# Kernel optimization log

Measured on AMD Instinct MI355X. Metric: run time of the kernel, lower is better.

Reference implementation:

```python
import jax, jax.numpy as jnp
import numpy as np

N, D, H, E, TOP_K = 8192, 1024, 2048, 8, 2


def setup_inputs() -> dict:
    key = jax.random.key(0)
    ks = jax.random.split(key, 5)
    s_in = 1.0 / np.sqrt(D)
    s_hid = 1.0 / np.sqrt(H)
    return {
        "x": jax.random.normal(ks[0], (N, D), dtype=jnp.float32),
        "Wg": jax.random.normal(ks[1], (D, E), dtype=jnp.float32) * s_in,
        "bg": jnp.zeros((E,), dtype=jnp.float32),
        "W1": jax.random.normal(ks[2], (E, D, H), dtype=jnp.float32) * s_in,
        "b1": jnp.zeros((E, H), dtype=jnp.float32),
        "W2": jax.random.normal(ks[3], (E, H, H), dtype=jnp.float32) * s_hid,
        "b2": jnp.zeros((E, H), dtype=jnp.float32),
    }


def _moe_forward(x, Wg, bg, W1, b1, W2, b2):
    # Router
    gate_logits = x @ Wg + bg                      # [N, E]
    gate_probs = jax.nn.softmax(gate_logits, axis=-1)
    topk_probs, topk_idx = jax.lax.top_k(gate_probs, TOP_K)  # [N, K]
    topk_probs = topk_probs / (jnp.sum(topk_probs, axis=-1, keepdims=True) + 1e-8)
    rows = jnp.arange(x.shape[0])[:, None]
    gate_mask = jnp.zeros_like(gate_probs).at[rows, topk_idx].set(topk_probs)  # [N, E]

    # Dense all-expert compute (dropout is identity in eval)
    h = jax.nn.relu(jnp.einsum('nd,edh->neh', x, W1) + b1)    # [N, E, H]
    expert_out = jnp.einsum('neh,ehk->nek', h, W2) + b2        # [N, E, H]

    output = jnp.einsum('neh,ne->nh', expert_out, gate_mask)   # [N, H]
    return output, gate_probs, gate_mask


def reference(x, Wg, bg, W1, b1, W2, b2):
    return _moe_forward(x, Wg, bg, W1, b1, W2, b2)
```

## Files before the change

### kernel.cpp

```cpp
#include <hip/hip_runtime.h>

#define N_TOK 8192
#define DIM   1024
#define HID   2048
#define NEXP  8
#define TOPK  2
#define BM 256
#define BN 256
#define BK 64
#define NTHREADS 512
#define MAXROWS (N_TOK*TOPK + NEXP*BM)
#define MAXRT   (MAXROWS/BM)
#define NT_COL  (HID/BN)
#define NPAIR   (N_TOK*TOPK)

typedef float f32x4 __attribute__((ext_vector_type(4)));
typedef short bf16x8 __attribute__((ext_vector_type(8)));

static __device__ __forceinline__ unsigned short f2bf(float f){
    union { float f; unsigned u; } v; v.f = f;
    unsigned r = v.u + 0x7FFFu + ((v.u >> 16) & 1u);
    return (unsigned short)(r >> 16);
}
static __device__ __forceinline__ float bf2f(unsigned short u){
    union { unsigned u; float f; } v; v.u = ((unsigned)u) << 16;
    return v.f;
}

static __device__ __forceinline__ void gload_lds16(const void* g, void* l){
    __builtin_amdgcn_global_load_lds((const __attribute__((address_space(1))) void*)g,
                                     (__attribute__((address_space(3))) void*)l,
                                     16, 0, 0);
}

__global__ __launch_bounds__(256) void cvt_transpose_moe(
    const float* __restrict__ src, unsigned short* __restrict__ dst, int R, int C)
{
    __shared__ float tile[64][65];
    const size_t plane = (size_t)R * C;
    const float* s = src + (size_t)blockIdx.z * plane;
    unsigned short* d = dst + (size_t)blockIdx.z * plane;
    const int c0 = blockIdx.x * 64, r0 = blockIdx.y * 64;
    const int tq = threadIdx.x & 15, tr = threadIdx.x >> 4;
    #pragma unroll
    for (int p = 0; p < 4; ++p) {
        int row = p*16 + tr;
        float4 v = *(const float4*)(s + (size_t)(r0 + row) * C + c0 + tq*4);
        tile[row][tq*4+0] = v.x; tile[row][tq*4+1] = v.y;
        tile[row][tq*4+2] = v.z; tile[row][tq*4+3] = v.w;
    }
    __syncthreads();
    #pragma unroll
    for (int p = 0; p < 4; ++p) {
        int orow = p*16 + tr;
        ushort4 o;
        o.x = f2bf(tile[tq*4+0][orow]);
        o.y = f2bf(tile[tq*4+1][orow]);
        o.z = f2bf(tile[tq*4+2][orow]);
        o.w = f2bf(tile[tq*4+3][orow]);
        *(ushort4*)(d + (size_t)(c0 + orow) * R + r0 + tq*4) = o;
    }
}

__global__ __launch_bounds__(256) void router_moe(
    const float* __restrict__ x, const float* __restrict__ Wg, const float* __restrict__ bg,
    float* __restrict__ gate_probs, float* __restrict__ gate_mask,
    int* __restrict__ tk_e, float* __restrict__ tk_w)
{
    const int lane = threadIdx.x & 63;
    const int n = blockIdx.x * 4 + (threadIdx.x >> 6);
    const float* xr = x + (size_t)n * DIM;

    float acc[NEXP];
    #pragma unroll
    for (int e = 0; e < NEXP; ++e) acc[e] = 0.f;
    #pragma unroll 4
    for (int i = 0; i < DIM/64; ++i) {
        int d = i*64 + lane;
        float xv = xr[d];
        const float4* wrow = (const float4*)(Wg + (size_t)d * NEXP);
        float4 w0 = wrow[0], w1 = wrow[1];
        acc[0] += xv*w0.x; acc[1] += xv*w0.y; acc[2] += xv*w0.z; acc[3] += xv*w0.w;
        acc[4] += xv*w1.x; acc[5] += xv*w1.y; acc[6] += xv*w1.z; acc[7] += xv*w1.w;
    }
    #pragma unroll
    for (int off = 32; off > 0; off >>= 1) {
        #pragma unroll
        for (int e = 0; e < NEXP; ++e) acc[e] += __shfl_xor(acc[e], off, 64);
    }
    float lgt[NEXP];
    float mx = acc[0] + bg[0];
    #pragma unroll
    for (int e = 0; e < NEXP; ++e) { lgt[e] = acc[e] + bg[e]; mx = fmaxf(mx, lgt[e]); }
    float s = 0.f;
    #pragma unroll
    for (int e = 0; e < NEXP; ++e) { lgt[e] = expf(lgt[e] - mx); s += lgt[e]; }
    float inv = 1.f / s;
    #pragma unroll
    for (int e = 0; e < NEXP; ++e) lgt[e] *= inv;

    int i1 = 0;
    #pragma unroll
    for (int e = 1; e < NEXP; ++e) if (lgt[e] > lgt[i1]) i1 = e;
    int i2 = (i1 == 0) ? 1 : 0;
    #pragma unroll
    for (int e = 0; e < NEXP; ++e) if (e != i1 && lgt[e] > lgt[i2]) i2 = e;
    float wsum = lgt[i1] + lgt[i2] + 1e-8f;
    float w1n = lgt[i1] / wsum, w2n = lgt[i2] / wsum;

    if (lane < NEXP) {
        gate_probs[(size_t)n*NEXP + lane] = lgt[lane];
        gate_mask [(size_t)n*NEXP + lane] = (lane == i1) ? w1n : (lane == i2) ? w2n : 0.f;
    }
    if (lane == 0) {
        tk_e[n*TOPK]   = i1; tk_e[n*TOPK+1] = i2;
        tk_w[n*TOPK]   = w1n; tk_w[n*TOPK+1] = w2n;
    }
}

__global__ __launch_bounds__(1024) void assign_moe(
    const int* __restrict__ tk_e,
    int* __restrict__ slot_row, int* __restrict__ pair_token,
    int* __restrict__ sched_e, int* __restrict__ sched_row,
    int* __restrict__ total_tiles)
{
    __shared__ int whist[16][NEXP];
    __shared__ int wbase[16][NEXP];
    const int w = threadIdx.x >> 6, lane = threadIdx.x & 63;
    const int PW = NPAIR / 16;
    const unsigned long long below = ((unsigned long long)1 << lane) - 1;

    int h[NEXP] = {0,0,0,0,0,0,0,0};
    for (int i = 0; i < PW/64; ++i) {
        int e = tk_e[w*PW + i*64 + lane];
        #pragma unroll
        for (int ee = 0; ee < NEXP; ++ee)
            h[ee] += __popcll(__ballot(e == ee));
    }
    if (lane == 0) {
        #pragma unroll
        for (int ee = 0; ee < NEXP; ++ee) whist[w][ee] = h[ee];
    }
    __syncthreads();

    if (threadIdx.x == 0) {
        int base = 0, t = 0, ebase[NEXP];
        for (int e = 0; e < NEXP; ++e) {
            int c = 0;
            for (int ww = 0; ww < 16; ++ww) c += whist[ww][e];
            ebase[e] = base;
            int nt = (c + BM - 1) / BM;
            for (int i = 0; i < nt; ++i) { sched_e[t] = e; sched_row[t] = base + i*BM; ++t; }
            base += nt * BM;
        }
        *total_tiles = t;
        for (int e = 0; e < NEXP; ++e) {
            int r = ebase[e];
            for (int ww = 0; ww < 16; ++ww) { wbase[ww][e] = r; r += whist[ww][e]; }
        }
    }
    __syncthreads();

    int run[NEXP];
    #pragma unroll
    for (int ee = 0; ee < NEXP; ++ee) run[ee] = wbase[w][ee];
    for (int i = 0; i < PW/64; ++i) {
        int idx = w*PW + i*64 + lane;
        int e = tk_e[idx];
        int myslot = 0;
        #pragma unroll
        for (int ee = 0; ee < NEXP; ++ee) {
            unsigned long long m = __ballot(e == ee);
            if (e == ee) myslot = run[ee] + __popcll(m & below);
            run[ee] += __popcll(m);
        }
        slot_row[idx] = myslot;
        pair_token[myslot] = idx;
    }
}

__global__ __launch_bounds__(256) void gather_moe(
    const float* __restrict__ x, const int* __restrict__ slot_row,
    unsigned short* __restrict__ Xg)
{
    const int n = blockIdx.x;
    const int r0 = slot_row[n*TOPK], r1 = slot_row[n*TOPK+1];
    float4 xv = ((const float4*)(x + (size_t)n * DIM))[threadIdx.x];
    ushort4 b;
    b.x = f2bf(xv.x); b.y = f2bf(xv.y); b.z = f2bf(xv.z); b.w = f2bf(xv.w);
    ((ushort4*)(Xg + (size_t)r0 * DIM))[threadIdx.x] = b;
    ((ushort4*)(Xg + (size_t)r1 * DIM))[threadIdx.x] = b;
}

#define PHASE_MFMA(MH, NH, BF) do {                                          \
    __builtin_amdgcn_s_setprio(1);                                           \
    _Pragma("unroll")                                                        \
    for (int mi = 0; mi < 4; ++mi)                                           \
        _Pragma("unroll")                                                    \
        for (int nb = 0; nb < 2; ++nb)                                       \
            _Pragma("unroll")                                                \
            for (int kk = 0; kk < 2; ++kk)                                   \
                acc[(MH)*4+mi][(NH)*2+nb] =                                  \
                    __builtin_amdgcn_mfma_f32_16x16x32_bf16(                 \
                        af[mi][kk], BF[nb][kk], acc[(MH)*4+mi][(NH)*2+nb],   \
                        0, 0, 0);                                            \
    __builtin_amdgcn_s_setprio(0);                                           \
} while (0)

template<int K, int MODE>
__global__ __launch_bounds__(512, 1) void gemm_moe(
    const unsigned short* __restrict__ A,
    const unsigned short* __restrict__ Bt,
    const float* __restrict__ bias,
    const int* __restrict__ sched_e, const int* __restrict__ sched_row,
    const int* __restrict__ total_tiles,
    unsigned short* __restrict__ Out,
    const int* __restrict__ pair_token)
{
    const int nwg  = gridDim.x * gridDim.y;
    const int orig = blockIdx.y * gridDim.x + blockIdx.x;
    const int q = nwg >> 3, r8 = nwg & 7, xcd = orig & 7, lin = orig >> 3;
    const int wg = (xcd < r8 ? xcd*(q+1) : r8*(q+1) + (xcd-r8)*q) + lin;
    const int rt = wg / NT_COL, ct = wg % NT_COL;
    if (rt >= *total_tiles) return;

    const int e    = sched_e[rt];
    const int row0 = sched_row[rt];
    const int col0 = ct * BN;
    const unsigned short* Be = Bt + (size_t)e * HID * K;

    __shared__ __align__(1024) char lds[131072];
    char* ldsA = lds;
    char* ldsB = lds + 65536;

    const int tid  = threadIdx.x;
    const int wv   = tid >> 6, lane = tid & 63;
    const int wr   = wv >> 2,  wc   = wv & 3;
    const int lrow = lane & 15, lg  = lane >> 4;
    const int sr   = lane >> 3, si  = lane & 7;
    const int gc16 = si ^ sr;

    const unsigned short* Ab = A  + (size_t)row0 * K + gc16 * 8;
    const unsigned short* Bb = Be + (size_t)col0 * K + gc16 * 8;

    f32x4 acc[8][4] = {};
    bf16x8 af[4][2], b0f[2][2], b1f[2][2];

    auto STAGE_A = [&](int buf, int h, int t) {
        char* dst = ldsA + (buf*2 + h)*16384;
        #pragma unroll
        for (int j = 0; j < 2; ++j) {
            int c = wv*2 + j;
            int r = ((c>>3)<<7) + h*64 + ((c&7)<<3) + sr;
            gload_lds16(Ab + (size_t)r * K + t*BK, dst + c*1024);
        }
    };
    auto STAGE_B = [&](int buf, int h, int t) {
        char* dst = ldsB + (buf*2 + h)*16384;
        #pragma unroll
        for (int j = 0; j < 2; ++j) {
            int c = wv*2 + j;
            int idx = c*8 + sr;
            int gcol = ((idx>>5)<<6) + h*32 + (idx&31);
            gload_lds16(Bb + (size_t)gcol * K + t*BK, dst + c*1024);
        }
    };
    auto RD_A = [&](int buf, int mh) {
        const char* base = ldsA + (buf*2 + mh)*16384;
        #pragma unroll
        for (int mi = 0; mi < 4; ++mi) {
            int idx = wr*64 + mi*16 + lrow;
            #pragma unroll
            for (int kk = 0; kk < 2; ++kk) {
                int s = (kk*4 + lg) ^ (idx & 7);
                af[mi][kk] = *(const bf16x8*)(base + idx*128 + s*16);
            }
        }
    };
    auto RD_B = [&](int buf, int nh, bf16x8 (*bf)[2]) {
        const char* base = ldsB + (buf*2 + nh)*16384;
        #pragma unroll
        for (int nb = 0; nb < 2; ++nb) {
            int idx = wc*32 + nb*16 + lrow;
            #pragma unroll
            for (int kk = 0; kk < 2; ++kk) {
                int s = (kk*4 + lg) ^ (idx & 7);
                bf[nb][kk] = *(const bf16x8*)(base + idx*128 + s*16);
            }
        }
    };
    auto BARRIER = [&]() {
        __builtin_amdgcn_sched_barrier(0);
        __builtin_amdgcn_s_barrier();
        __builtin_amdgcn_sched_barrier(0);
    };
    auto LGKM0 = [&]() {
        asm volatile("s_waitcnt lgkmcnt(0)" ::: "memory");
        __builtin_amdgcn_sched_barrier(0);
    };

    constexpr int NT = K / BK;
    constexpr int NI = NT / 2;
    static_assert(NT % 2 == 0, "even K-tiles required");

    STAGE_A(0,0,0); STAGE_B(0,0,0); STAGE_A(0,1,0); STAGE_B(0,1,0);
    STAGE_A(1,0,1); STAGE_B(1,0,1);
    asm volatile("s_waitcnt vmcnt(4)" ::: "memory");
    BARRIER();

    for (int i = 0; i < NI; ++i) {
        const int ta = 2*i, tb = 2*i + 1;
        const bool pf = (i + 1 < NI);
        RD_A(0,0); RD_B(0,0,b0f);
        STAGE_A(1,1,tb);
        BARRIER(); LGKM0();
        PHASE_MFMA(0,0,b0f);
        BARRIER();
        RD_B(0,1,b1f);
        STAGE_B(1,1,tb);
        BARRIER(); LGKM0();
        PHASE_MFMA(0,1,b1f);
        BARRIER();
        RD_A(0,1);
        if (pf) STAGE_A(0,0,ta+2);
        BARRIER(); LGKM0();
        PHASE_MFMA(1,0,b0f);
        BARRIER();
        if (pf) STAGE_B(0,0,ta+2);
        BARRIER();
        PHASE_MFMA(1,1,b1f);
        if (pf) { asm volatile("s_waitcnt vmcnt(4)" ::: "memory"); }
        else    { asm volatile("s_waitcnt vmcnt(0)" ::: "memory"); }
        BARRIER();
        RD_A(1,0); RD_B(1,0,b0f);
        if (pf) STAGE_A(0,1,ta+2);
        BARRIER(); LGKM0();
        PHASE_MFMA(0,0,b0f);
        BARRIER();
        RD_B(1,1,b1f);
        if (pf) STAGE_B(0,1,ta+2);
        BARRIER(); LGKM0();
        PHASE_MFMA(0,1,b1f);
        BARRIER();
        RD_A(1,1);
        if (pf) STAGE_A(1,0,tb+2);
        BARRIER(); LGKM0();
        PHASE_MFMA(1,0,b0f);
        BARRIER();
        if (pf) STAGE_B(1,0,tb+2);
        BARRIER();
        PHASE_MFMA(1,1,b1f);
        if (pf) { asm volatile("s_waitcnt vmcnt(4)" ::: "memory"); BARRIER(); }
    }

    if constexpr (MODE == 0) {
        #pragma unroll
        for (int nb = 0; nb < 4; ++nb) {
            int col = col0 + wc*64 + nb*16 + lrow;
            float bv = bias[(size_t)e*HID + col];
            #pragma unroll
            for (int mb = 0; mb < 8; ++mb) {
                int rb = row0 + wr*128 + mb*16 + lg*4;
                #pragma unroll
                for (int j = 0; j < 4; ++j) {
                    float v = fmaxf(acc[mb][nb][j] + bv, 0.f);
                    Out[(size_t)(rb + j) * HID + col] = f2bf(v);
                }
            }
        }
    } else {
        float bv[4]; int cols[4];
        #pragma unroll
        for (int nb = 0; nb < 4; ++nb) {
            cols[nb] = col0 + wc*64 + nb*16 + lrow;
            bv[nb] = bias[(size_t)e*HID + cols[nb]];
        }
        #pragma unroll
        for (int mb = 0; mb < 8; ++mb) {
            #pragma unroll
            for (int j = 0; j < 4; ++j) {
                int r = row0 + wr*128 + mb*16 + lg*4 + j;
                int pair = pair_token[r];
                if (pair < 0) continue;
                size_t prow = (size_t)(pair & 1) * N_TOK + (pair >> 1);
                #pragma unroll
                for (int nb = 0; nb < 4; ++nb)
                    Out[prow * HID + cols[nb]] = f2bf(acc[mb][nb][j] + bv[nb]);
            }
        }
    }
}

__global__ __launch_bounds__(256) void combine_moe(
    const unsigned short* __restrict__ P, const float* __restrict__ tk_w,
    float* __restrict__ out)
{
    const int n = blockIdx.x;
    const float w0 = tk_w[n*2], w1 = tk_w[n*2+1];
    const int c = threadIdx.x * 8;
    bf16x8 a = *(const bf16x8*)(P + (size_t)n * HID + c);
    bf16x8 b = *(const bf16x8*)(P + (size_t)(N_TOK + n) * HID + c);
    float4 o0, o1;
    float* op = &o0.x;
    #pragma unroll
    for (int i = 0; i < 4; ++i)
        op[i] = w0 * bf2f((unsigned short)a[i]) + w1 * bf2f((unsigned short)b[i]);
    float* op1 = &o1.x;
    #pragma unroll
    for (int i = 0; i < 4; ++i)
        op1[i] = w0 * bf2f((unsigned short)a[4+i]) + w1 * bf2f((unsigned short)b[4+i]);
    float4* dst = (float4*)(out + (size_t)n * HID + c);
    dst[0] = o0; dst[1] = o1;
}

extern "C" void kernel_launch(void* const* d_in, const int* in_sizes, int n_in,
                              void* d_out, int out_size, void* d_ws, size_t ws_size,
                              hipStream_t stream)
{
    const float* x  = (const float*)d_in[0];
    const float* Wg = (const float*)d_in[1];
    const float* bg = (const float*)d_in[2];
    const float* W1 = (const float*)d_in[3];
    const float* b1 = (const float*)d_in[4];
    const float* W2 = (const float*)d_in[5];
    const float* b2 = (const float*)d_in[6];

    float* out        = (float*)d_out;
    float* gate_probs = out + (size_t)N_TOK * HID;
    float* gate_mask  = gate_probs + (size_t)N_TOK * NEXP;

    char* p = (char*)d_ws;
    auto carve = [&](size_t bytes) { char* r = p; p += (bytes + 255) & ~(size_t)255; return r; };
    unsigned short* W2t = (unsigned short*)carve((size_t)NEXP*HID*HID*2);
    unsigned short* Hb  = (unsigned short*)carve((size_t)MAXROWS*HID*2);
    unsigned short* W1t = (unsigned short*)carve((size_t)NEXP*DIM*HID*2);
    unsigned short* Xg  = (unsigned short*)carve((size_t)MAXROWS*DIM*2);
    unsigned short* P   = W1t;
    int*   pair_token = (int*)  carve((size_t)MAXROWS*4);
    int*   slot_row   = (int*)  carve((size_t)NPAIR*4);
    int*   tk_e       = (int*)  carve((size_t)NPAIR*4);
    float* tk_w       = (float*)carve((size_t)NPAIR*4);
    int*   sched_e    = (int*)  carve(1024);
    int*   sched_row  = (int*)  carve(1024);
    int*   total_tiles= (int*)  carve(256);

    hipMemsetAsync(pair_token, 0xFF, (size_t)MAXROWS*4, stream);

    cvt_transpose_moe<<<dim3(HID/64, DIM/64, NEXP), 256, 0, stream>>>(W1, W1t, DIM, HID);
    cvt_transpose_moe<<<dim3(HID/64, HID/64, NEXP), 256, 0, stream>>>(W2, W2t, HID, HID);
    router_moe<<<N_TOK/4, 256, 0, stream>>>(x, Wg, bg, gate_probs, gate_mask, tk_e, tk_w);
    assign_moe<<<1, 1024, 0, stream>>>(tk_e, slot_row, pair_token,
                                       sched_e, sched_row, total_tiles);
    gather_moe<<<N_TOK, 256, 0, stream>>>(x, slot_row, Xg);
    gemm_moe<DIM, 0><<<dim3(MAXRT, NT_COL), NTHREADS, 0, stream>>>(
        Xg, W1t, b1, sched_e, sched_row, total_tiles, Hb, nullptr);
    gemm_moe<HID, 1><<<dim3(MAXRT, NT_COL), NTHREADS, 0, stream>>>(
        Hb, W2t, b2, sched_e, sched_row, total_tiles, P, pair_token);
    combine_moe<<<N_TOK, 256, 0, stream>>>(P, tk_w, out);
}
```

Baseline: 398.5 us.

## Split first expert GEMM into dedicated 256x128-tile kernel with two blocks per CU

```diff
diff --git a/kernel.cpp b/kernel.cpp
--- a/kernel.cpp
+++ b/kernel.cpp
@@ -6,12 +6,10 @@
 #define NEXP  8
 #define TOPK  2
 #define BM 256
-#define BN 256
 #define BK 64
 #define NTHREADS 512
 #define MAXROWS (N_TOK*TOPK + NEXP*BM)
 #define MAXRT   (MAXROWS/BM)
-#define NT_COL  (HID/BN)
 #define NPAIR   (N_TOK*TOPK)
 
 typedef float f32x4 __attribute__((ext_vector_type(4)));
@@ -192,7 +190,164 @@
     ((ushort4*)(Xg + (size_t)r1 * DIM))[threadIdx.x] = b;
 }
 
-#define PHASE_MFMA(MH, NH, BF) do {                                          \
+#define G1_BN 128
+#define G1_NTCOL (HID/G1_BN)
+
+#define G1_MFMA(MH, NH, BF) do {                                             \
+    __builtin_amdgcn_s_setprio(1);                                           \
+    _Pragma("unroll")                                                        \
+    for (int mi = 0; mi < 2; ++mi)                                           \
+        _Pragma("unroll")                                                    \
+        for (int nb = 0; nb < 2; ++nb)                                       \
+            _Pragma("unroll")                                                \
+            for (int kk = 0; kk < 2; ++kk)                                   \
+                acc[(MH)*2+mi][(NH)*2+nb] =                                  \
+                    __builtin_amdgcn_mfma_f32_16x16x32_bf16(                 \
+                        af[mi][kk], BF[nb][kk], acc[(MH)*2+mi][(NH)*2+nb],   \
+                        0, 0, 0);                                            \
+    __builtin_amdgcn_s_setprio(0);                                           \
+} while (0)
+
+__global__ __launch_bounds__(512, 2) void gemm1_moe(
+    const unsigned short* __restrict__ A,
+    const unsigned short* __restrict__ Bt,
+    const float* __restrict__ bias,
+    const int* __restrict__ sched_e, const int* __restrict__ sched_row,
+    const int* __restrict__ total_tiles,
+    unsigned short* __restrict__ Out)
+{
+    constexpr int K = DIM;
+    const int nwg  = gridDim.x * gridDim.y;
+    const int orig = blockIdx.y * gridDim.x + blockIdx.x;
+    const int q = nwg >> 3, r8 = nwg & 7, xcd = orig & 7, lin = orig >> 3;
+    const int wg = (xcd < r8 ? xcd*(q+1) : r8*(q+1) + (xcd-r8)*q) + lin;
+    const int rt = wg / G1_NTCOL, ct = wg % G1_NTCOL;
+    if (rt >= *total_tiles) return;
+
+    const int e    = sched_e[rt];
+    const int row0 = sched_row[rt];
+    const int col0 = ct * G1_BN;
+    const unsigned short* Be = Bt + (size_t)e * HID * K;
+
+    __shared__ __align__(1024) char lds[49152];
+    char* ldsA = lds;
+    char* ldsB = lds + 32768;
+
+    const int tid  = threadIdx.x;
+    const int wv   = tid >> 6, lane = tid & 63;
+    const int wr   = wv >> 1,  wc   = wv & 1;
+    const int lrow = lane & 15, lg  = lane >> 4;
+    const int sr   = lane >> 3, si  = lane & 7;
+    const int gc16 = si ^ sr;
+
+    const unsigned short* Ab = A  + (size_t)row0 * K + gc16 * 8;
+    const unsigned short* Bb = Be + (size_t)col0 * K + gc16 * 8;
+
+    f32x4 acc[4][4] = {};
+    bf16x8 af[2][2], b0f[2][2], b1f[2][2];
+
+    auto STAGE_A = [&](int h, int t) {
+        char* dst = ldsA + h*16384;
+        #pragma unroll
+        for (int j = 0; j < 2; ++j) {
+            int c = wv*2 + j;
+            int idx = c*8 + sr;
+            int r = ((idx>>5)<<6) + h*32 + (idx&31);
+            gload_lds16(Ab + (size_t)r * K + t*BK, dst + c*1024);
+        }
+    };
+    auto STAGE_B = [&](int h, int t) {
+        char* dst = ldsB + h*8192;
+        int c = wv;
+        int idx = c*8 + sr;
+        int gcol = ((idx>>5)<<6) + h*32 + (idx&31);
+        gload_lds16(Bb + (size_t)gcol * K + t*BK, dst + c*1024);
+    };
+    auto RD_A = [&](int mh) {
+        const char* base = ldsA + mh*16384;
+        #pragma unroll
+        for (int mi = 0; mi < 2; ++mi) {
+            int idx = wr*32 + mi*16 + lrow;
+            #pragma unroll
+            for (int kk = 0; kk < 2; ++kk) {
+                int s = (kk*4 + lg) ^ (idx & 7);
+                af[mi][kk] = *(const bf16x8*)(base + idx*128 + s*16);
+            }
+        }
+    };
+    auto RD_B = [&](int nh, bf16x8 (*bf)[2]) {
+        const char* base = ldsB + nh*8192;
+        #pragma unroll
+        for (int nb = 0; nb < 2; ++nb) {
+            int idx = wc*32 + nb*16 + lrow;
+            #pragma unroll
+            for (int kk = 0; kk < 2; ++kk) {
+                int s = (kk*4 + lg) ^ (idx & 7);
+                bf[nb][kk] = *(const bf16x8*)(base + idx*128 + s*16);
+            }
+        }
+    };
+    auto BARRIER = [&]() {
+        __builtin_amdgcn_sched_barrier(0);
+        __builtin_amdgcn_s_barrier();
+        __builtin_amdgcn_sched_barrier(0);
+    };
+    auto LGKM0 = [&]() {
+        asm volatile("s_waitcnt lgkmcnt(0)" ::: "memory");
+        __builtin_amdgcn_sched_barrier(0);
+    };
+
+    constexpr int NT = K / BK;
+
+    STAGE_A(0, 0); STAGE_B(0, 0); STAGE_B(1, 0); STAGE_A(1, 0);
+    asm volatile("s_waitcnt vmcnt(3)" ::: "memory");
+    BARRIER();
+
+    for (int t = 0; t < NT; ++t) {
+        const bool pf = (t + 1 < NT);
+        RD_A(0); RD_B(0, b0f);
+        BARRIER(); LGKM0();
+        G1_MFMA(0,0,b0f);
+        asm volatile("s_waitcnt vmcnt(2)" ::: "memory");
+        BARRIER();
+        RD_B(1, b1f);
+        if (pf) { STAGE_A(0, t+1); STAGE_B(0, t+1); }
+        BARRIER(); LGKM0();
+        G1_MFMA(0,1,b1f);
+        if (pf) { asm volatile("s_waitcnt vmcnt(3)" ::: "memory"); }
+        else    { asm volatile("s_waitcnt vmcnt(0)" ::: "memory"); }
+        BARRIER();
+        RD_A(1);
+        if (pf) STAGE_B(1, t+1);
+        BARRIER(); LGKM0();
+        G1_MFMA(1,0,b0f);
+        BARRIER();
+        if (pf) STAGE_A(1, t+1);
+        BARRIER();
+        G1_MFMA(1,1,b1f);
+        if (pf) { asm volatile("s_waitcnt vmcnt(3)" ::: "memory"); BARRIER(); }
+    }
+
+    #pragma unroll
+    for (int n = 0; n < 4; ++n) {
+        int col = col0 + wc*64 + ((n>>1)<<5) + ((n&1)<<4) + lrow;
+        float bv = bias[(size_t)e*HID + col];
+        #pragma unroll
+        for (int m = 0; m < 4; ++m) {
+            int rb = row0 + wr*64 + ((m>>1)<<5) + ((m&1)<<4) + lg*4;
+            #pragma unroll
+            for (int j = 0; j < 4; ++j) {
+                float v = fmaxf(acc[m][n][j] + bv, 0.f);
+                Out[(size_t)(rb + j) * HID + col] = f2bf(v);
+            }
+        }
+    }
+}
+
+#define G2_BN 256
+#define G2_NTCOL (HID/G2_BN)
+
+#define G2_MFMA(MH, NH, BF) do {                                             \
     __builtin_amdgcn_s_setprio(1);                                           \
     _Pragma("unroll")                                                        \
     for (int mi = 0; mi < 4; ++mi)                                           \
@@ -207,8 +362,7 @@
     __builtin_amdgcn_s_setprio(0);                                           \
 } while (0)
 
-template<int K, int MODE>
-__global__ __launch_bounds__(512, 1) void gemm_moe(
+__global__ __launch_bounds__(512, 1) void gemm2_moe(
     const unsigned short* __restrict__ A,
     const unsigned short* __restrict__ Bt,
     const float* __restrict__ bias,
@@ -217,16 +371,17 @@
     unsigned short* __restrict__ Out,
     const int* __restrict__ pair_token)
 {
+    constexpr int K = HID;
     const int nwg  = gridDim.x * gridDim.y;
     const int orig = blockIdx.y * gridDim.x + blockIdx.x;
     const int q = nwg >> 3, r8 = nwg & 7, xcd = orig & 7, lin = orig >> 3;
     const int wg = (xcd < r8 ? xcd*(q+1) : r8*(q+1) + (xcd-r8)*q) + lin;
-    const int rt = wg / NT_COL, ct = wg % NT_COL;
+    const int rt = wg / G2_NTCOL, ct = wg % G2_NTCOL;
     if (rt >= *total_tiles) return;
 
     const int e    = sched_e[rt];
     const int row0 = sched_row[rt];
-    const int col0 = ct * BN;
+    const int col0 = ct * G2_BN;
     const unsigned short* Be = Bt + (size_t)e * HID * K;
 
     __shared__ __align__(1024) char lds[131072];
@@ -314,79 +469,62 @@
         RD_A(0,0); RD_B(0,0,b0f);
         STAGE_A(1,1,tb);
         BARRIER(); LGKM0();
-        PHASE_MFMA(0,0,b0f);
+        G2_MFMA(0,0,b0f);
         BARRIER();
         RD_B(0,1,b1f);
         STAGE_B(1,1,tb);
         BARRIER(); LGKM0();
-        PHASE_MFMA(0,1,b1f);
+        G2_MFMA(0,1,b1f);
         BARRIER();
         RD_A(0,1);
         if (pf) STAGE_A(0,0,ta+2);
         BARRIER(); LGKM0();
-        PHASE_MFMA(1,0,b0f);
+        G2_MFMA(1,0,b0f);
         BARRIER();
         if (pf) STAGE_B(0,0,ta+2);
         BARRIER();
-        PHASE_MFMA(1,1,b1f);
+        G2_MFMA(1,1,b1f);
         if (pf) { asm volatile("s_waitcnt vmcnt(4)" ::: "memory"); }
         else    { asm volatile("s_waitcnt vmcnt(0)" ::: "memory"); }
         BARRIER();
         RD_A(1,0); RD_B(1,0,b0f);
         if (pf) STAGE_A(0,1,ta+2);
         BARRIER(); LGKM0();
-        PHASE_MFMA(0,0,b0f);
+        G2_MFMA(0,0,b0f);
         BARRIER();
         RD_B(1,1,b1f);
         if (pf) STAGE_B(0,1,ta+2);
         BARRIER(); LGKM0();
-        PHASE_MFMA(0,1,b1f);
+        G2_MFMA(0,1,b1f);
         BARRIER();
         RD_A(1,1);
         if (pf) STAGE_A(1,0,tb+2);
         BARRIER(); LGKM0();
-        PHASE_MFMA(1,0,b0f);
+        G2_MFMA(1,0,b0f);
         BARRIER();
         if (pf) STAGE_B(1,0,tb+2);
         BARRIER();
-        PHASE_MFMA(1,1,b1f);
+        G2_MFMA(1,1,b1f);
         if (pf) { asm volatile("s_waitcnt vmcnt(4)" ::: "memory"); BARRIER(); }
     }
 
-    if constexpr (MODE == 0) {
-        #pragma unroll
-        for (int nb = 0; nb < 4; ++nb) {
-            int col = col0 + wc*64 + nb*16 + lrow;
-            float bv = bias[(size_t)e*HID + col];
+    float bv[4]; int cols[4];
+    #pragma unroll
+    for (int nb = 0; nb < 4; ++nb) {
+        cols[nb] = col0 + wc*64 + nb*16 + lrow;
+        bv[nb] = bias[(size_t)e*HID + cols[nb]];
+    }
+    #pragma unroll
+    for (int mb = 0; mb < 8; ++mb) {
+        #pragma unroll
+        for (int j = 0; j < 4; ++j) {
+            int r = row0 + wr*128 + mb*16 + lg*4 + j;
+            int pair = pair_token[r];
+            if (pair < 0) continue;
+            size_t prow = (size_t)(pair & 1) * N_TOK + (pair >> 1);
             #pragma unroll
-            for (int mb = 0; mb < 8; ++mb) {
-                int rb = row0 + wr*128 + mb*16 + lg*4;
-                #pragma unroll
-                for (int j = 0; j < 4; ++j) {
-                    float v = fmaxf(acc[mb][nb][j] + bv, 0.f);
-                    Out[(size_t)(rb + j) * HID + col] = f2bf(v);
-                }
-            }
-        }
-    } else {
-        float bv[4]; int cols[4];
-        #pragma unroll
-        for (int nb = 0; nb < 4; ++nb) {
-            cols[nb] = col0 + wc*64 + nb*16 + lrow;
-            bv[nb] = bias[(size_t)e*HID + cols[nb]];
-        }
-        #pragma unroll
-        for (int mb = 0; mb < 8; ++mb) {
-            #pragma unroll
-            for (int j = 0; j < 4; ++j) {
-                int r = row0 + wr*128 + mb*16 + lg*4 + j;
-                int pair = pair_token[r];
-                if (pair < 0) continue;
-                size_t prow = (size_t)(pair & 1) * N_TOK + (pair >> 1);
-                #pragma unroll
-                for (int nb = 0; nb < 4; ++nb)
-                    Out[prow * HID + cols[nb]] = f2bf(acc[mb][nb][j] + bv[nb]);
-            }
+            for (int nb = 0; nb < 4; ++nb)
+                Out[prow * HID + cols[nb]] = f2bf(acc[mb][nb][j] + bv[nb]);
         }
     }
 }
@@ -452,9 +590,9 @@
     assign_moe<<<1, 1024, 0, stream>>>(tk_e, slot_row, pair_token,
                                        sched_e, sched_row, total_tiles);
     gather_moe<<<N_TOK, 256, 0, stream>>>(x, slot_row, Xg);
-    gemm_moe<DIM, 0><<<dim3(MAXRT, NT_COL), NTHREADS, 0, stream>>>(
-        Xg, W1t, b1, sched_e, sched_row, total_tiles, Hb, nullptr);
-    gemm_moe<HID, 1><<<dim3(MAXRT, NT_COL), NTHREADS, 0, stream>>>(
+    gemm1_moe<<<dim3(MAXRT, G1_NTCOL), NTHREADS, 0, stream>>>(
+        Xg, W1t, b1, sched_e, sched_row, total_tiles, Hb);
+    gemm2_moe<<<dim3(MAXRT, G2_NTCOL), NTHREADS, 0, stream>>>(
         Hb, W2t, b2, sched_e, sched_row, total_tiles, P, pair_token);
     combine_moe<<<N_TOK, 256, 0, stream>>>(P, tk_w, out);
 }
```

Result: faster. 382.6 us (-4.0%).
